# Kernel tuning notes

Measured on AMD Instinct MI355X. Metric: run time of the kernel, lower is better.

## Reference

```python
import jax, jax.numpy as jnp
import numpy as np

N_NODES = 100000
N_EDGES = 1600000
D_IN, D_HID, D_OUT = 128, 128, 64


def spmm(row, col, val, h, n):
    # y[i] = sum_{e: row[e]==i} val[e] * h[col[e]]  (A_hat @ h with A in COO form)
    return jax.ops.segment_sum(val[:, None] * h[col], row, num_segments=n)


def setup_inputs() -> dict:
    key = jax.random.key(0)
    ks = jax.random.split(key, 7)
    x = jax.random.normal(ks[0], (1, N_NODES, D_IN), dtype=jnp.float32)
    edge_row = jax.random.randint(ks[1], (N_EDGES,), 0, N_NODES, dtype=jnp.int32)
    edge_col = jax.random.randint(ks[2], (N_EDGES,), 0, N_NODES, dtype=jnp.int32)
    edge_val = jax.random.uniform(ks[3], (N_EDGES,), dtype=jnp.float32)
    W0 = jax.random.normal(ks[4], (D_HID, D_IN), dtype=jnp.float32) * 0.05
    W1 = jax.random.normal(ks[5], (D_HID, D_HID), dtype=jnp.float32) * 0.05
    W2 = jax.random.normal(ks[6], (D_OUT, D_HID), dtype=jnp.float32) * 0.05
    return {"x": x, "edge_row": edge_row, "edge_col": edge_col,
            "edge_val": edge_val, "W0": W0, "W1": W1, "W2": W2}


def reference(x, edge_row, edge_col, edge_val, W0, W1, W2):
    B, N, D = x.shape
    n = B * N
    h = x.reshape(n, D)
    # input conv: Linear (no bias) -> SpMM -> ReLU
    h = jax.nn.relu(spmm(edge_row, edge_col, edge_val, h @ W0.T, n))
    # hidden conv with residual: ReLU(A (h W1^T)) + h
    h = jax.nn.relu(spmm(edge_row, edge_col, edge_val, h @ W1.T, n)) + h
    # dropout is identity in eval mode
    out = spmm(edge_row, edge_col, edge_val, h @ W2.T, n)
    return out
```

## Files before the change

### kernel.cpp

```cpp
#include <hip/hip_runtime.h>


typedef unsigned int u32;
typedef unsigned short u16;
typedef __attribute__((ext_vector_type(8))) short bf16x8;
typedef __attribute__((ext_vector_type(4))) float f32x4;

constexpr int NN = 100000;
constexpr int NE = 1600000;
constexpr int PAD = 100352;
constexpr int NBUCK = 392;
constexpr int BCAP = 4608;
constexpr int EPB = 8192;
constexpr int P1B = (NE + EPB - 1) / EPB;
constexpr int G0B = (NN + 63) / 64;
constexpr int NCB = 13;

__device__ __forceinline__ u16 f2bf(float f) {
    u32 x = __float_as_uint(f);
    x += 0x7fffu + ((x >> 16) & 1u);
    return (u16)(x >> 16);
}

__device__ __forceinline__ void wfrag_one(const float* __restrict__ W,
                                          u16* __restrict__ Wf, int total, int i)
{
    if (i < total) {
        const int j    = i & 7;
        const int lane = (i >> 3) & 63;
        const int kc   = (i >> 9) & 3;
        const int ct   = i >> 11;
        const int src  = (ct * 16 + (lane & 15)) * 128 + kc * 32 + (lane >> 4) * 8 + j;
        Wf[i] = f2bf(W[src]);
    }
}

__global__ __launch_bounds__(256)
void wcvt_kernel(const float* __restrict__ W0, const float* __restrict__ W1,
                 const float* __restrict__ W2, u16* __restrict__ wf0,
                 u16* __restrict__ wf1, u16* __restrict__ wf2,
                 int* __restrict__ bcur)
{
    const int i = blockIdx.x * 256 + threadIdx.x;
    if (i < 512) bcur[i] = 0;
    wfrag_one(W0, wf0, 128 * 128, i);
    wfrag_one(W1, wf1, 128 * 128, i);
    wfrag_one(W2, wf2, 64 * 128, i);
}

__global__ __launch_bounds__(256)
void k1_kernel(const float* __restrict__ x, const u16* __restrict__ Wf,
               u16* __restrict__ Cb,
               const int* __restrict__ erow, const int* __restrict__ ecol,
               const float* __restrict__ eval, int* __restrict__ bcur,
               int2* __restrict__ part, int* __restrict__ boffs)
{
    __shared__ u16 smem[64 * 136];
    const int tid = threadIdx.x;

    if ((int)blockIdx.x < P1B) {
        int* shist = (int*)smem;
        int* sexcl = shist + 512;
        int* sdat  = sexcl + 512;
        const int blk = blockIdx.x;
        shist[tid] = 0; shist[tid + 256] = 0;
        __syncthreads();

        const int base = blk * EPB;
        #pragma unroll
        for (int j = 0; j < EPB / 256; ++j) {
            const int e = base + j * 256 + tid;
            if (e < NE) atomicAdd(&shist[erow[e] >> 8], 1);
        }
        __syncthreads();

        const int c0 = shist[2 * tid];
        const int c1 = shist[2 * tid + 1];
        if (c0) atomicAdd(&bcur[2 * tid], c0);
        if (c1) atomicAdd(&bcur[2 * tid + 1], c1);
        const int tsum = c0 + c1;
        sdat[tid] = tsum;
        __syncthreads();
        #pragma unroll
        for (int off = 1; off < 256; off <<= 1) {
            const int v = (tid >= off) ? sdat[tid - off] : 0;
            __syncthreads();
            sdat[tid] += v;
            __syncthreads();
        }
        const int excl = sdat[tid] - tsum;
        sexcl[2 * tid]     = excl;
        sexcl[2 * tid + 1] = excl + c0;
        const int total = sdat[255];
        __syncthreads();

        for (int b = tid; b < NBUCK; b += 256)
            boffs[(size_t)b * P1B + blk] = sexcl[b];
        if (tid == 0) boffs[(size_t)NBUCK * P1B + blk] = total;

        #pragma unroll
        for (int j = 0; j < EPB / 256; ++j) {
            const int e = base + j * 256 + tid;
            if (e < NE) {
                const int r = erow[e];
                const int b = r >> 8;
                const int pos = atomicAdd(&sexcl[b], 1);
                part[(size_t)blk * EPB + pos] =
                    make_int2(((r & 255) << 17) | ecol[e], __float_as_int(eval[e]));
            }
        }
        return;
    }

    constexpr int RS   = 136;
    constexpr int PADW = 136;
    u16* sA = smem;
    u16* sC = smem;
    const int w    = tid >> 6;
    const int lane = tid & 63;
    const int m    = lane & 15;
    const int q    = lane >> 4;
    const int rowBase = ((int)blockIdx.x - P1B) * 64;

    #pragma unroll
    for (int i = 0; i < 8; ++i) {
        const int g = (i * 256 + tid) * 4;
        const int r = g >> 7, c = g & 127;
        float4 v = make_float4(0.f, 0.f, 0.f, 0.f);
        if (rowBase + r < NN) v = *(const float4*)(x + (size_t)(rowBase + r) * 128 + c);
        u16* d = &sA[r * RS + c];
        d[0] = f2bf(v.x); d[1] = f2bf(v.y); d[2] = f2bf(v.z); d[3] = f2bf(v.w);
    }
    __syncthreads();

    bf16x8 afrag[4];
    #pragma unroll
    for (int kc = 0; kc < 4; ++kc)
        afrag[kc] = *(const bf16x8*)&sA[(w * 16 + m) * RS + kc * 32 + q * 8];
    __syncthreads();

    #pragma unroll
    for (int ct = 0; ct < 8; ++ct) {
        f32x4 acc = {0.f, 0.f, 0.f, 0.f};
        #pragma unroll
        for (int kc = 0; kc < 4; ++kc) {
            const bf16x8 b = *(const bf16x8*)(Wf + (((ct * 4 + kc) * 64) + lane) * 8);
            acc = __builtin_amdgcn_mfma_f32_16x16x32_bf16(afrag[kc], b, acc, 0, 0, 0);
        }
        #pragma unroll
        for (int r = 0; r < 4; ++r)
            sC[(w * 16 + q * 4 + r) * PADW + ct * 16 + m] = f2bf(acc[r]);
    }
    __syncthreads();

    const int g    = lane >> 2;
    const int cb   = (lane & 3) * 32;
    const int grow = rowBase + w * 16 + g;
    if (grow < NN) {
        #pragma unroll
        for (int i = 0; i < 4; ++i) {
            const int4 v = *(const int4*)&sC[(w * 16 + g) * PADW + cb + i * 8];
            *(int4*)(Cb + (size_t)grow * 128 + cb + i * 8) = v;
        }
    }
}

__global__ __launch_bounds__(256)
void part2_kernel(const int* __restrict__ bcur, const int* __restrict__ boffs,
                  const int2* __restrict__ part,
                  int* __restrict__ offs, int2* __restrict__ pce)
{
    __shared__ int2 sbuf[BCAP];
    __shared__ int scnt[256 * NCB];
    __shared__ int sdata[256];
    const int b = blockIdx.x;
    const int tid = threadIdx.x;

    int partial = 0;
    for (int i = tid; i < b; i += 256) partial += bcur[i];
    sdata[tid] = partial;
    __syncthreads();
    #pragma unroll
    for (int off = 128; off > 0; off >>= 1) {
        if (tid < off) sdata[tid] += sdata[tid + off];
        __syncthreads();
    }
    const int gb = sdata[0];
    const int cnt = bcur[b];
    __syncthreads();

    int lo = 0, len = 0;
    if (tid < P1B) {
        lo  = boffs[(size_t)b * P1B + tid];
        len = boffs[(size_t)(b + 1) * P1B + tid] - lo;
    }
    sdata[tid] = len;
    __syncthreads();
    #pragma unroll
    for (int off = 1; off < 256; off <<= 1) {
        const int v = (tid >= off) ? sdata[tid - off] : 0;
        __syncthreads();
        sdata[tid] += v;
        __syncthreads();
    }
    const int dst = sdata[tid] - len;

    #pragma unroll
    for (int j = 0; j < NCB; ++j) scnt[j * 256 + tid] = 0;

    if (tid < P1B && len > 0) {
        const int2* srcp = part + (size_t)tid * EPB + lo;
        for (int i = 0; i < len; ++i) sbuf[dst + i] = srcp[i];
    }
    __syncthreads();

    for (int i = tid; i < cnt; i += 256) {
        const int xk = sbuf[i].x;
        atomicAdd(&scnt[(((u32)xk) >> 17) * NCB + ((xk & 0x1FFFF) >> 13)], 1);
    }
    __syncthreads();

    int rsum = 0;
    #pragma unroll
    for (int j = 0; j < NCB; ++j) rsum += scnt[tid * NCB + j];
    sdata[tid] = rsum;
    __syncthreads();
    #pragma unroll
    for (int off = 1; off < 256; off <<= 1) {
        const int v = (tid >= off) ? sdata[tid - off] : 0;
        __syncthreads();
        sdata[tid] += v;
        __syncthreads();
    }
    const int excl = sdata[tid] - rsum;
    offs[b * 256 + tid] = gb + excl;

    int run = gb + excl;
    #pragma unroll
    for (int j = 0; j < NCB; ++j) {
        const int c = scnt[tid * NCB + j];
        scnt[tid * NCB + j] = run;
        run += c;
    }
    __syncthreads();

    for (int i = tid; i < cnt; i += 256) {
        const int2 ev = sbuf[i];
        const int rl = ((u32)ev.x) >> 17;
        const int cb = (ev.x & 0x1FFFF) >> 13;
        const int pos = atomicAdd(&scnt[rl * NCB + cb], 1);
        pce[pos] = make_int2(ev.x & 0x1FFFF, ev.y);
    }
}

template<int LPC>
__device__ __forceinline__ void load_row(const u16* p, u32* u) {
    if constexpr (LPC == 8) {
        const uint4 t = *(const uint4*)p;
        u[0] = t.x; u[1] = t.y; u[2] = t.z; u[3] = t.w;
    } else {
        const uint2 t = *(const uint2*)p;
        u[0] = t.x; u[1] = t.y;
    }
}

template<int LPC>
__device__ __forceinline__ void fma_row(float v, const u32* u, float* a) {
    #pragma unroll
    for (int j = 0; j < LPC / 2; ++j) {
        a[2*j]   = fmaf(v, __uint_as_float(u[j] << 16),         a[2*j]);
        a[2*j+1] = fmaf(v, __uint_as_float(u[j] & 0xffff0000u), a[2*j+1]);
    }
}

template<int DO, int MODE>
__global__ __launch_bounds__(256)
void spmm_gemm(const int* __restrict__ offs, const int2* __restrict__ pce,
               const u16* __restrict__ Hb, const u16* __restrict__ Wf,
               const u16* __restrict__ Res, u16* __restrict__ Cb,
               u16* __restrict__ Hout)
{
    constexpr int RS   = 136;
    constexpr int PADW = DO + 8;
    __shared__ u16 smem[16 * 136];
    const int tid = threadIdx.x;
    const int ln  = tid & 15;
    const int rl  = tid >> 4;
    const int row = blockIdx.x * 16 + rl;

    const int s = offs[row];
    const int t = offs[row + 1];
    const u16* hbase = Hb + ln * 8;

    float a0[8], a1[8];
    #pragma unroll
    for (int j = 0; j < 8; ++j) { a0[j] = 0.f; a1[j] = 0.f; }

    for (int e = s; e < t; e += 16) {
        int2 my = make_int2(0, 0);
        if (e + ln < t) my = pce[e + ln];
        const int rem = t - e;
        #pragma unroll
        for (int qd = 0; qd < 4; ++qd) {
            if (qd * 4 < rem) {
                const int c0 = __shfl(my.x, qd * 4 + 0, 16);
                const int v0 = __shfl(my.y, qd * 4 + 0, 16);
                const int c1 = __shfl(my.x, qd * 4 + 1, 16);
                const int v1 = __shfl(my.y, qd * 4 + 1, 16);
                const int c2 = __shfl(my.x, qd * 4 + 2, 16);
                const int v2 = __shfl(my.y, qd * 4 + 2, 16);
                const int c3 = __shfl(my.x, qd * 4 + 3, 16);
                const int v3 = __shfl(my.y, qd * 4 + 3, 16);
                u32 u0[4], u1[4], u2[4], u3[4];
                load_row<8>(hbase + (size_t)c0 * 128, u0);
                load_row<8>(hbase + (size_t)c1 * 128, u1);
                load_row<8>(hbase + (size_t)c2 * 128, u2);
                load_row<8>(hbase + (size_t)c3 * 128, u3);
                fma_row<8>(__int_as_float(v0), u0, a0);
                fma_row<8>(__int_as_float(v1), u1, a1);
                fma_row<8>(__int_as_float(v2), u2, a0);
                fma_row<8>(__int_as_float(v3), u3, a1);
            }
        }
    }
    #pragma unroll
    for (int j = 0; j < 8; ++j) a0[j] = fmaxf(a0[j] + a1[j], 0.f);

    if constexpr (MODE == 2) {
        u32 r[4];
        load_row<8>(Res + (size_t)row * 128 + ln * 8, r);
        #pragma unroll
        for (int j = 0; j < 4; ++j) {
            a0[2*j]   += __uint_as_float(r[j] << 16);
            a0[2*j+1] += __uint_as_float(r[j] & 0xffff0000u);
        }
    }
    u32 o[4];
    #pragma unroll
    for (int j = 0; j < 4; ++j)
        o[j] = (u32)f2bf(a0[2*j]) | ((u32)f2bf(a0[2*j+1]) << 16);
    const uint4 packed = make_uint4(o[0], o[1], o[2], o[3]);
    *(uint4*)&smem[rl * RS + ln * 8] = packed;
    if constexpr (MODE == 1)
        *(uint4*)(Hout + (size_t)row * 128 + ln * 8) = packed;
    __syncthreads();

    constexpr int TPW = DO / 64;
    const int w    = tid >> 6;
    const int lane = tid & 63;
    const int m    = lane & 15;
    const int q    = lane >> 4;

    bf16x8 afrag[4];
    #pragma unroll
    for (int kc = 0; kc < 4; ++kc)
        afrag[kc] = *(const bf16x8*)&smem[m * RS + kc * 32 + q * 8];

    f32x4 acc[TPW];
    #pragma unroll
    for (int tw = 0; tw < TPW; ++tw) {
        const int ct = w * TPW + tw;
        acc[tw] = (f32x4){0.f, 0.f, 0.f, 0.f};
        #pragma unroll
        for (int kc = 0; kc < 4; ++kc) {
            const bf16x8 b = *(const bf16x8*)(Wf + (((ct * 4 + kc) * 64) + lane) * 8);
            acc[tw] = __builtin_amdgcn_mfma_f32_16x16x32_bf16(afrag[kc], b, acc[tw], 0, 0, 0);
        }
    }
    __syncthreads();

    #pragma unroll
    for (int tw = 0; tw < TPW; ++tw) {
        const int ct = w * TPW + tw;
        #pragma unroll
        for (int r = 0; r < 4; ++r)
            smem[(q * 4 + r) * PADW + ct * 16 + m] = f2bf(acc[tw][r]);
    }
    __syncthreads();

    if (DO == 128 || tid < 128) {
        const int g = tid * 8;
        const int r = g / DO;
        const int c = g % DO;
        const int4 v = *(const int4*)&smem[r * PADW + c];
        *(int4*)(Cb + ((size_t)blockIdx.x * 16 + r) * DO + c) = v;
    }
}

__global__ __launch_bounds__(256)
void spmm_out(const int* __restrict__ offs, const int2* __restrict__ pce,
              const u16* __restrict__ Hb, float* __restrict__ Y)
{
    const int ln  = threadIdx.x & 15;
    const int row = blockIdx.x * 16 + (threadIdx.x >> 4);
    if (row >= NN) return;
    const int s = offs[row];
    const int t = offs[row + 1];
    const u16* hbase = Hb + ln * 4;

    float a0[4], a1[4];
    #pragma unroll
    for (int j = 0; j < 4; ++j) { a0[j] = 0.f; a1[j] = 0.f; }

    for (int e = s; e < t; e += 16) {
        int2 my = make_int2(0, 0);
        if (e + ln < t) my = pce[e + ln];
        const int rem = t - e;
        #pragma unroll
        for (int qd = 0; qd < 4; ++qd) {
            if (qd * 4 < rem) {
                const int c0 = __shfl(my.x, qd * 4 + 0, 16);
                const int v0 = __shfl(my.y, qd * 4 + 0, 16);
                const int c1 = __shfl(my.x, qd * 4 + 1, 16);
                const int v1 = __shfl(my.y, qd * 4 + 1, 16);
                const int c2 = __shfl(my.x, qd * 4 + 2, 16);
                const int v2 = __shfl(my.y, qd * 4 + 2, 16);
                const int c3 = __shfl(my.x, qd * 4 + 3, 16);
                const int v3 = __shfl(my.y, qd * 4 + 3, 16);
                u32 u0[2], u1[2], u2[2], u3[2];
                load_row<4>(hbase + (size_t)c0 * 64, u0);
                load_row<4>(hbase + (size_t)c1 * 64, u1);
                load_row<4>(hbase + (size_t)c2 * 64, u2);
                load_row<4>(hbase + (size_t)c3 * 64, u3);
                fma_row<4>(__int_as_float(v0), u0, a0);
                fma_row<4>(__int_as_float(v1), u1, a1);
                fma_row<4>(__int_as_float(v2), u2, a0);
                fma_row<4>(__int_as_float(v3), u3, a1);
            }
        }
    }
    #pragma unroll
    for (int j = 0; j < 4; ++j) a0[j] += a1[j];
    *(float4*)(Y + (size_t)row * 64 + ln * 4) = make_float4(a0[0], a0[1], a0[2], a0[3]);
}

extern "C" void kernel_launch(void* const* d_in, const int* in_sizes, int n_in,
                              void* d_out, int out_size, void* d_ws, size_t ws_size,
                              hipStream_t stream) {
    const float* x    = (const float*)d_in[0];
    const int*   erow = (const int*)  d_in[1];
    const int*   ecol = (const int*)  d_in[2];
    const float* eval = (const float*)d_in[3];
    const float* W0   = (const float*)d_in[4];
    const float* W1   = (const float*)d_in[5];
    const float* W2   = (const float*)d_in[6];
    float* out = (float*)d_out;

    char* p = (char*)d_ws;
    const size_t BUFB = (size_t)NN * 128 * sizeof(u16);
    u16* t0b  = (u16*)p;  p += BUFB;
    u16* t1b  = (u16*)p;  p += BUFB;
    u16* h1b  = (u16*)p;  p += BUFB;
    u16* wf0  = (u16*)p;  p += 128 * 128 * 2;
    u16* wf1  = (u16*)p;  p += 128 * 128 * 2;
    u16* wf2  = (u16*)p;  p += 64 * 128 * 2;
    int* bcur   = (int*)p; p += 512 * 4;
    int* boffs  = (int*)p; p += (size_t)(NBUCK + 1) * P1B * 4;
    int* offs   = (int*)p; p += ((size_t)PAD + 256) * 4;
    int2* part  = (int2*)p; p += (size_t)P1B * EPB * 8;
    int2* pce   = (int2*)p;

    const dim3 blk(256);
    const int rowBlocks = NN / 16;

    wcvt_kernel<<<64, blk, 0, stream>>>(W0, W1, W2, wf0, wf1, wf2, bcur);
    k1_kernel  <<<P1B + G0B, blk, 0, stream>>>(x, wf0, t0b, erow, ecol, eval, bcur, part, boffs);
    part2_kernel<<<NBUCK, blk, 0, stream>>>(bcur, boffs, part, offs, pce);
    spmm_gemm<128, 1><<<rowBlocks, blk, 0, stream>>>(offs, pce, t0b, wf1, nullptr, t1b, h1b);
    spmm_gemm<64, 2><<<rowBlocks, blk, 0, stream>>>(offs, pce, t1b, wf2, h1b, t0b, nullptr);
    spmm_out<<<rowBlocks, blk, 0, stream>>>(offs, pce, t0b, out);
}
```

Before: 331.0 us.

## Split partition from GEMM, halve edges per block, parallelize bucket gather

```diff
diff --git a/kernel.cpp b/kernel.cpp
--- a/kernel.cpp
+++ b/kernel.cpp
@@ -11,7 +11,7 @@
 constexpr int PAD = 100352;
 constexpr int NBUCK = 392;
 constexpr int BCAP = 4608;
-constexpr int EPB = 8192;
+constexpr int EPB = 4096;
 constexpr int P1B = (NE + EPB - 1) / EPB;
 constexpr int G0B = (NN + 63) / 64;
 constexpr int NCB = 13;
@@ -38,89 +38,87 @@
 __global__ __launch_bounds__(256)
 void wcvt_kernel(const float* __restrict__ W0, const float* __restrict__ W1,
                  const float* __restrict__ W2, u16* __restrict__ wf0,
-                 u16* __restrict__ wf1, u16* __restrict__ wf2,
-                 int* __restrict__ bcur)
+                 u16* __restrict__ wf1, u16* __restrict__ wf2)
 {
     const int i = blockIdx.x * 256 + threadIdx.x;
-    if (i < 512) bcur[i] = 0;
     wfrag_one(W0, wf0, 128 * 128, i);
     wfrag_one(W1, wf1, 128 * 128, i);
     wfrag_one(W2, wf2, 64 * 128, i);
 }
 
 __global__ __launch_bounds__(256)
-void k1_kernel(const float* __restrict__ x, const u16* __restrict__ Wf,
-               u16* __restrict__ Cb,
-               const int* __restrict__ erow, const int* __restrict__ ecol,
-               const float* __restrict__ eval, int* __restrict__ bcur,
-               int2* __restrict__ part, int* __restrict__ boffs)
-{
-    __shared__ u16 smem[64 * 136];
+void part1_kernel(const int* __restrict__ erow, const int* __restrict__ ecol,
+                  const float* __restrict__ eval,
+                  int2* __restrict__ part, int* __restrict__ boffs)
+{
+    __shared__ int shist[512];
+    __shared__ int sexcl[512];
+    __shared__ int sdat[256];
     const int tid = threadIdx.x;
-
-    if ((int)blockIdx.x < P1B) {
-        int* shist = (int*)smem;
-        int* sexcl = shist + 512;
-        int* sdat  = sexcl + 512;
-        const int blk = blockIdx.x;
-        shist[tid] = 0; shist[tid + 256] = 0;
-        __syncthreads();
-
-        const int base = blk * EPB;
-        #pragma unroll
-        for (int j = 0; j < EPB / 256; ++j) {
+    const int blk = blockIdx.x;
+
+    shist[tid] = 0; shist[tid + 256] = 0;
+    __syncthreads();
+
+    const int base = blk * EPB;
+    int rr[EPB / 256];
+    #pragma unroll
+    for (int j = 0; j < EPB / 256; ++j) {
+        const int e = base + j * 256 + tid;
+        rr[j] = (e < NE) ? erow[e] : -1;
+        if (rr[j] >= 0) atomicAdd(&shist[rr[j] >> 8], 1);
+    }
+    __syncthreads();
+
+    const int c0 = shist[2 * tid];
+    const int c1 = shist[2 * tid + 1];
+    const int tsum = c0 + c1;
+    sdat[tid] = tsum;
+    __syncthreads();
+    #pragma unroll
+    for (int off = 1; off < 256; off <<= 1) {
+        const int v = (tid >= off) ? sdat[tid - off] : 0;
+        __syncthreads();
+        sdat[tid] += v;
+        __syncthreads();
+    }
+    const int excl = sdat[tid] - tsum;
+    sexcl[2 * tid]     = excl;
+    sexcl[2 * tid + 1] = excl + c0;
+    __syncthreads();
+
+    for (int b = tid; b < NBUCK; b += 256)
+        boffs[(size_t)b * P1B + blk] = sexcl[b];
+    if (tid == 0) boffs[(size_t)NBUCK * P1B + blk] = sdat[255];
+    __syncthreads();
+
+    #pragma unroll
+    for (int j = 0; j < EPB / 256; ++j) {
+        const int r = rr[j];
+        if (r >= 0) {
             const int e = base + j * 256 + tid;
-            if (e < NE) atomicAdd(&shist[erow[e] >> 8], 1);
-        }
-        __syncthreads();
-
-        const int c0 = shist[2 * tid];
-        const int c1 = shist[2 * tid + 1];
-        if (c0) atomicAdd(&bcur[2 * tid], c0);
-        if (c1) atomicAdd(&bcur[2 * tid + 1], c1);
-        const int tsum = c0 + c1;
-        sdat[tid] = tsum;
-        __syncthreads();
-        #pragma unroll
-        for (int off = 1; off < 256; off <<= 1) {
-            const int v = (tid >= off) ? sdat[tid - off] : 0;
-            __syncthreads();
-            sdat[tid] += v;
-            __syncthreads();
-        }
-        const int excl = sdat[tid] - tsum;
-        sexcl[2 * tid]     = excl;
-        sexcl[2 * tid + 1] = excl + c0;
-        const int total = sdat[255];
-        __syncthreads();
-
-        for (int b = tid; b < NBUCK; b += 256)
-            boffs[(size_t)b * P1B + blk] = sexcl[b];
-        if (tid == 0) boffs[(size_t)NBUCK * P1B + blk] = total;
-
-        #pragma unroll
-        for (int j = 0; j < EPB / 256; ++j) {
-            const int e = base + j * 256 + tid;
-            if (e < NE) {
-                const int r = erow[e];
-                const int b = r >> 8;
-                const int pos = atomicAdd(&sexcl[b], 1);
-                part[(size_t)blk * EPB + pos] =
-                    make_int2(((r & 255) << 17) | ecol[e], __float_as_int(eval[e]));
-            }
-        }
-        return;
-    }
-
+            const int pos = atomicAdd(&sexcl[r >> 8], 1);
+            part[(size_t)blk * EPB + pos] =
+                make_int2(((r & 255) << 17) | ecol[e], __float_as_int(eval[e]));
+        }
+    }
+}
+
+__global__ __launch_bounds__(256)
+void gemm0_kernel(const float* __restrict__ x, const u16* __restrict__ Wf,
+                  u16* __restrict__ Cb)
+{
     constexpr int RS   = 136;
     constexpr int PADW = 136;
+    __shared__ u16 smem[64 * 136];
     u16* sA = smem;
     u16* sC = smem;
+    const int tid  = threadIdx.x;
     const int w    = tid >> 6;
     const int lane = tid & 63;
     const int m    = lane & 15;
     const int q    = lane >> 4;
-    const int rowBase = ((int)blockIdx.x - P1B) * 64;
+    const int rowBase = (int)blockIdx.x * 64;
 
     #pragma unroll
     for (int i = 0; i < 8; ++i) {
@@ -166,12 +164,33 @@
 }
 
 __global__ __launch_bounds__(256)
+void bsum_kernel(const int* __restrict__ boffs, int* __restrict__ bcur)
+{
+    __shared__ int sdata[256];
+    const int b = blockIdx.x;
+    const int tid = threadIdx.x;
+    int s = 0;
+    for (int k = tid; k < P1B; k += 256)
+        s += boffs[(size_t)(b + 1) * P1B + k] - boffs[(size_t)b * P1B + k];
+    sdata[tid] = s;
+    __syncthreads();
+    #pragma unroll
+    for (int off = 128; off > 0; off >>= 1) {
+        if (tid < off) sdata[tid] += sdata[tid + off];
+        __syncthreads();
+    }
+    if (tid == 0) bcur[b] = sdata[0];
+}
+
+__global__ __launch_bounds__(256)
 void part2_kernel(const int* __restrict__ bcur, const int* __restrict__ boffs,
                   const int2* __restrict__ part,
                   int* __restrict__ offs, int2* __restrict__ pce)
 {
     __shared__ int2 sbuf[BCAP];
     __shared__ int scnt[256 * NCB];
+    __shared__ int slo[512];
+    __shared__ int sinc[512];
     __shared__ int sdata[256];
     const int b = blockIdx.x;
     const int tid = threadIdx.x;
@@ -189,28 +208,43 @@
     const int cnt = bcur[b];
     __syncthreads();
 
-    int lo = 0, len = 0;
-    if (tid < P1B) {
-        lo  = boffs[(size_t)b * P1B + tid];
-        len = boffs[(size_t)(b + 1) * P1B + tid] - lo;
-    }
-    sdata[tid] = len;
-    __syncthreads();
-    #pragma unroll
-    for (int off = 1; off < 256; off <<= 1) {
-        const int v = (tid >= off) ? sdata[tid - off] : 0;
-        __syncthreads();
-        sdata[tid] += v;
-        __syncthreads();
-    }
-    const int dst = sdata[tid] - len;
-
+    {
+        int k = tid;
+        int l0 = 0, ln = 0;
+        if (k < P1B) {
+            l0 = boffs[(size_t)b * P1B + k];
+            ln = boffs[(size_t)(b + 1) * P1B + k] - l0;
+        }
+        slo[k] = l0; sinc[k] = ln;
+        k = tid + 256; l0 = 0; ln = 0;
+        if (k < P1B) {
+            l0 = boffs[(size_t)b * P1B + k];
+            ln = boffs[(size_t)(b + 1) * P1B + k] - l0;
+        }
+        slo[k] = l0; sinc[k] = ln;
+    }
     #pragma unroll
     for (int j = 0; j < NCB; ++j) scnt[j * 256 + tid] = 0;
-
-    if (tid < P1B && len > 0) {
-        const int2* srcp = part + (size_t)tid * EPB + lo;
-        for (int i = 0; i < len; ++i) sbuf[dst + i] = srcp[i];
+    __syncthreads();
+
+    for (int off = 1; off < 512; off <<= 1) {
+        const int v0 = (tid >= off) ? sinc[tid - off] : 0;
+        const int v1 = (tid + 256 >= off) ? sinc[tid + 256 - off] : 0;
+        __syncthreads();
+        sinc[tid]       += v0;
+        sinc[tid + 256] += v1;
+        __syncthreads();
+    }
+
+    for (int i = tid; i < cnt; i += 256) {
+        int k = 0;
+        #pragma unroll
+        for (int step = 256; step > 0; step >>= 1) {
+            const int nk = k + step;
+            if (nk <= 511 && sinc[nk - 1] <= i) k = nk;
+        }
+        const int loc = i - (k ? sinc[k - 1] : 0);
+        sbuf[i] = part[(size_t)k * EPB + slo[k] + loc];
     }
     __syncthreads();
 
@@ -246,9 +280,8 @@
 
     for (int i = tid; i < cnt; i += 256) {
         const int2 ev = sbuf[i];
-        const int rl = ((u32)ev.x) >> 17;
-        const int cb = (ev.x & 0x1FFFF) >> 13;
-        const int pos = atomicAdd(&scnt[rl * NCB + cb], 1);
+        const int pos = atomicAdd(
+            &scnt[(((u32)ev.x) >> 17) * NCB + ((ev.x & 0x1FFFF) >> 13)], 1);
         pce[pos] = make_int2(ev.x & 0x1FFFF, ev.y);
     }
 }
@@ -463,8 +496,10 @@
     const dim3 blk(256);
     const int rowBlocks = NN / 16;
 
-    wcvt_kernel<<<64, blk, 0, stream>>>(W0, W1, W2, wf0, wf1, wf2, bcur);
-    k1_kernel  <<<P1B + G0B, blk, 0, stream>>>(x, wf0, t0b, erow, ecol, eval, bcur, part, boffs);
+    wcvt_kernel <<<64, blk, 0, stream>>>(W0, W1, W2, wf0, wf1, wf2);
+    part1_kernel<<<P1B, blk, 0, stream>>>(erow, ecol, eval, part, boffs);
+    gemm0_kernel<<<G0B, blk, 0, stream>>>(x, wf0, t0b);
+    bsum_kernel <<<NBUCK, blk, 0, stream>>>(boffs, bcur);
     part2_kernel<<<NBUCK, blk, 0, stream>>>(bcur, boffs, part, offs, pce);
     spmm_gemm<128, 1><<<rowBlocks, blk, 0, stream>>>(offs, pce, t0b, wf1, nullptr, t1b, h1b);
     spmm_gemm<64, 2><<<rowBlocks, blk, 0, stream>>>(offs, pce, t1b, wf2, h1b, t0b, nullptr);
```

Result: slower. 337.8 us (+2.1%).
